# Optimization experiments

Hardware: AMD Instinct MI355X
Metric: run time of the kernel (lower is better)

The kernel has to match this reference:

```python
import jax, jax.numpy as jnp
import numpy as np

VERY_SMOL_NUM = -1e9  # undefined global in source; interpreted as large negative mask value
D_K = 128


def setup_inputs() -> dict:
    key = jax.random.key(0)
    k1, k2, k3 = jax.random.split(key, 3)
    B, S, D = 16, 2048, D_K
    Q = jax.random.normal(k1, (B, S, D), dtype=jnp.float32)
    K = jax.random.normal(k2, (B, S, D), dtype=jnp.float32)
    V = jax.random.normal(k3, (B, S, D), dtype=jnp.float32)
    return {"Q": Q, "K": K, "V": V}


def reference(Q, K, V):
    B, S, d_k = Q.shape
    # scores: [B, S, S] = Q @ K^T, scaled by 1/sqrt(d_k)
    x = jnp.einsum("bqd,bkd->bqk", Q, K) / jnp.sqrt(jnp.asarray(d_k, Q.dtype))
    # mask() is called unconditionally in the source (masked=False -> applied once):
    # add strict upper-triangular VERY_SMOL_NUM
    tri = jnp.triu(jnp.ones((S, S), dtype=x.dtype), k=1) * jnp.asarray(VERY_SMOL_NUM, x.dtype)
    x = x + tri  # broadcasts over batch, matching torch.triu on full shape
    # Softmax over dim=1 (query axis), as in the source (torch.nn.Softmax(dim=1))
    x = jax.nn.softmax(x, axis=1)
    return jnp.einsum("bqk,bkd->bqd", x, V)
```

## Files before the change

### kernel.cpp

```cpp
#include <hip/hip_runtime.h>


#define B_ 16
#define S_ 2048
#define D_ 128
#define QSCALE 0.12751744416825963f
#define NEG_BIG -1e30f
#define NCH 16
#define CHQ 128
#define PB 2162688

#define ROWW 136
#define P2RW 24

#define LDS_BARRIER()                                  \
  do {                                                 \
    asm volatile("s_waitcnt lgkmcnt(0)" ::: "memory"); \
    __builtin_amdgcn_s_barrier();                      \
  } while (0)

typedef short bf16x8 __attribute__((ext_vector_type(8)));
typedef float f32x4 __attribute__((ext_vector_type(4)));
typedef unsigned short u16x4 __attribute__((ext_vector_type(4)));
typedef unsigned int u32x2 __attribute__((ext_vector_type(2)));

#if defined(__has_builtin)
#if __has_builtin(__builtin_amdgcn_exp2f)
#define EXP2F(x) __builtin_amdgcn_exp2f(x)
#endif
#endif
#ifndef EXP2F
extern "C" __device__ float __ocml_exp2_f32(float);
#define EXP2F(x) __ocml_exp2_f32(x)
#endif

static __device__ __forceinline__ unsigned short f2bf(float f) {
  unsigned int u = __builtin_bit_cast(unsigned int, f);
  u += 0x7FFFu + ((u >> 16) & 1u);
  return (unsigned short)(u >> 16);
}

__global__ __launch_bounds__(256) void sdpa_convert(
    const float* __restrict__ Qr, const float* __restrict__ Kr,
    unsigned short* __restrict__ Qb, unsigned short* __restrict__ Kb) {
  const size_t t = (size_t)blockIdx.x * 256 + threadIdx.x;
  const float* src = blockIdx.y ? Kr : Qr;
  unsigned short* dstp = blockIdx.y ? Kb : Qb;
  const float sc = blockIdx.y ? 1.0f : QSCALE;
  f32x4 x = ((const f32x4*)src)[t];
  u16x4 o;
#pragma unroll
  for (int j = 0; j < 4; ++j) o[j] = f2bf(x[j] * sc);
  ((u16x4*)dstp)[t] = o;
}

__global__ __launch_bounds__(256, 4) void sdpa_pass1(
    const short* __restrict__ Qb, const short* __restrict__ Kb,
    float* __restrict__ lp_ws, unsigned short* __restrict__ Pt) {
  const int bid = blockIdx.x;
  int j = bid >> 4;
  int g = 0;
  while (j >= NCH - g) {
    j -= NCH - g;
    ++g;
  }
  const int ci = g + j;
  const int b = (bid & 7) + 8 * ((bid >> 3) & 1);

  __shared__ __align__(16) short Qst[2][32 * ROWW];
  const int tid = threadIdx.x;
  const int w = tid >> 6, lane = tid & 63, quad = lane >> 4, l15 = lane & 15;
  const int gg = 2 * g + (w >> 1);
  const int gb = 64 * gg;
  const int kb = gb + (w & 1) * 32;

  const size_t koff = ((size_t)b * S_ + kb + l15) * D_ + quad * 8;
  bf16x8 kh0[4], kh1[4];
#pragma unroll
  for (int c = 0; c < 4; ++c) {
    kh0[c] = *(const bf16x8*)(Kb + koff + c * 32);
    kh1[c] = *(const bf16x8*)(Kb + koff + 16 * D_ + c * 32);
  }

  const int nrp = S_ - gb;
  const size_t grp =
      (size_t)4 * ((size_t)gg * S_ - (size_t)(32 * gg) * (gg - 1));
  unsigned short* pw0 = Pt + (size_t)b * PB +
                        16 * (grp + (size_t)(2 * (w & 1)) * nrp) + quad * 4;
  unsigned short* pw1 = pw0 + (size_t)16 * nrp;

  const int sr = tid >> 3, sseg = tid & 7;
  const int q_start = CHQ * ci;

  {
    const short* sq = Qb + ((size_t)(b * S_ + q_start + sr)) * D_ + sseg * 16;
    bf16x8 h0 = *(const bf16x8*)(sq), h1 = *(const bf16x8*)(sq + 8);
    short* dst = &Qst[0][sr * ROWW + sseg * 16];
    *(bf16x8*)(dst) = h0;
    *(bf16x8*)(dst + 8) = h1;
  }
  LDS_BARRIER();

#define EMIT(q0s_, ktb_, cA_, pw_, lp_)                                       \
  do {                                                                        \
    float s0_ = cA_[0], s1_ = cA_[1], s2_ = cA_[2], s3_ = cA_[3];             \
    if ((q0s_) < (ktb_) + 16) {              \
      const int q_ = (q0s_) + l15;                                            \
      if ((ktb_) + quad * 4 + 0 > q_) s0_ = NEG_BIG;                          \
      if ((ktb_) + quad * 4 + 1 > q_) s1_ = NEG_BIG;                          \
      if ((ktb_) + quad * 4 + 2 > q_) s2_ = NEG_BIG;                          \
      if ((ktb_) + quad * 4 + 3 > q_) s3_ = NEG_BIG;                          \
    }                                                                         \
    const float e0_ = EXP2F(s0_), e1_ = EXP2F(s1_);                           \
    const float e2_ = EXP2F(s2_), e3_ = EXP2F(s3_);                           \
    lp_[0] += e0_;                                                            \
    lp_[1] += e1_;                                                            \
    lp_[2] += e2_;                                                            \
    lp_[3] += e3_;                                                            \
    unsigned int w0_, w1_;                                                    \
    asm("v_cvt_pk_bf16_f32 %0, %1, %2" : "=v"(w0_) : "v"(e0_), "v"(e1_));     \
    asm("v_cvt_pk_bf16_f32 %0, %1, %2" : "=v"(w1_) : "v"(e2_), "v"(e3_));     \
    u32x2 pk2_ = {w0_, w1_};                                                  \
    *(u32x2*)((pw_) + (size_t)((q0s_)-gb + l15) * 16) = pk2_;                 \
  } while (0)

  f32x4 lp0 = {0.f, 0.f, 0.f, 0.f}, lp1 = {0.f, 0.f, 0.f, 0.f};
#pragma unroll
  for (int it = 0; it < 4; ++it) {
    const int q0 = q_start + it * 32;
    const int cur = it & 1;
    bf16x8 h0, h1;
    if (it < 3) {
      const short* sq =
          Qb + ((size_t)(b * S_ + q0 + 32 + sr)) * D_ + sseg * 16;
      h0 = *(const bf16x8*)(sq);
      h1 = *(const bf16x8*)(sq + 8);
    }
#pragma unroll
    for (int sub = 0; sub < 2; ++sub) {
      const int q0s = q0 + sub * 16;
      if (q0s >= gb) {
        const short* rowp = &Qst[cur][(sub * 16 + l15) * ROWW + quad * 8];
        bf16x8 q0v = *(const bf16x8*)(rowp);
        bf16x8 q1v = *(const bf16x8*)(rowp + 32);
        bf16x8 q2v = *(const bf16x8*)(rowp + 64);
        bf16x8 q3v = *(const bf16x8*)(rowp + 96);
        f32x4 c0 = {0.f, 0.f, 0.f, 0.f};
        f32x4 c1 = {0.f, 0.f, 0.f, 0.f};
        c0 = __builtin_amdgcn_mfma_f32_16x16x32_bf16(kh0[0], q0v, c0, 0, 0, 0);
        c1 = __builtin_amdgcn_mfma_f32_16x16x32_bf16(kh1[0], q0v, c1, 0, 0, 0);
        c0 = __builtin_amdgcn_mfma_f32_16x16x32_bf16(kh0[1], q1v, c0, 0, 0, 0);
        c1 = __builtin_amdgcn_mfma_f32_16x16x32_bf16(kh1[1], q1v, c1, 0, 0, 0);
        c0 = __builtin_amdgcn_mfma_f32_16x16x32_bf16(kh0[2], q2v, c0, 0, 0, 0);
        c1 = __builtin_amdgcn_mfma_f32_16x16x32_bf16(kh1[2], q2v, c1, 0, 0, 0);
        c0 = __builtin_amdgcn_mfma_f32_16x16x32_bf16(kh0[3], q3v, c0, 0, 0, 0);
        c1 = __builtin_amdgcn_mfma_f32_16x16x32_bf16(kh1[3], q3v, c1, 0, 0, 0);
        EMIT(q0s, kb, c0, pw0, lp0);
        EMIT(q0s, kb + 16, c1, pw1, lp1);
      }
    }
    if (it < 3) {
      short* dst = &Qst[1 - cur][sr * ROWW + sseg * 16];
      *(bf16x8*)(dst) = h0;
      *(bf16x8*)(dst + 8) = h1;
    }
    LDS_BARRIER();
  }
#undef EMIT

#pragma unroll
  for (int d = 1; d < 16; d <<= 1) {
#pragma unroll
    for (int r = 0; r < 4; ++r) {
      lp0[r] += __shfl_xor(lp0[r], d, 64);
      lp1[r] += __shfl_xor(lp1[r], d, 64);
    }
  }
  if (l15 == 0) {
    float* dst = lp_ws + ((size_t)b * NCH + ci) * S_ + kb;
    *(f32x4*)(dst + quad * 4) = lp0;
    *(f32x4*)(dst + 16 + quad * 4) = lp1;
  }
}

__global__ __launch_bounds__(256) void sdpa_vscale(
    const float* __restrict__ Vr, const float* __restrict__ lp_ws,
    unsigned short* __restrict__ Vf) {
  __shared__ float Vld[32][132];
  __shared__ float as[32];
  const int kt = blockIdx.x, b = blockIdx.y, tid = threadIdx.x;
  const int k0 = kt * 32;
  const int row = tid >> 3, seg = tid & 7;
  const float* src = Vr + ((size_t)(b * S_ + k0 + row)) * D_ + seg * 16;
#pragma unroll
  for (int j = 0; j < 4; ++j) {
    f32x4 x = *(const f32x4*)(src + 4 * j);
    *(f32x4*)&Vld[row][seg * 16 + 4 * j] = x;
  }
  if (tid < 32) {
    const int k = k0 + tid;
    const int first = k >> 7;
    float l = 0.f;
#pragma unroll
    for (int ci = 0; ci < NCH; ++ci)
      if (ci >= first) l += lp_ws[((size_t)b * NCH + ci) * S_ + k];
    as[tid] = 1.0f / l;
  }
  __syncthreads();
  unsigned short* dst = Vf + ((size_t)(b * 64 + kt)) * 4096 + (size_t)tid * 16;
#pragma unroll
  for (int i = 0; i < 2; ++i) {
    const int u = tid * 2 + i;
    const int dt = u >> 6, l15 = (u >> 2) & 15, quad = u & 3;
    bf16x8 o;
#pragma unroll
    for (int e = 0; e < 8; ++e) {
      const int k = quad * 8 + e;
      o[e] = (short)f2bf(Vld[k][dt * 16 + l15] * as[k]);
    }
    *(bf16x8*)(dst + i * 8) = o;
  }
}

__global__ __launch_bounds__(512, 2) void sdpa_pass2(
    const unsigned short* __restrict__ Pt,
    const unsigned short* __restrict__ Vf, float* __restrict__ Out) {
  __shared__ __align__(16) short Pst[2][4 * 64 * P2RW];
  __shared__ __align__(16) short Vst[2][8192];
  const int bid = blockIdx.x;
  const int b = (bid & 7) + 8 * ((bid >> 3) & 1);
  const int py = bid >> 4;
  const int tid = threadIdx.x;
  const int w = tid >> 6, lane = tid & 63, quad = lane >> 4, l15 = lane & 15;
  const int qh = w & 3;
  const int dh = w >> 2;

  const int sp = tid >> 7, su = tid & 127, srow = su >> 1, sh = su & 1;

  const int ard = ((quad >> 1) * 64 + 16 * qh + l15) * P2RW + (quad & 1) * 8;
  const int awr = (sp * 64 + srow) * P2RW + sh * 8;
  const int vrd = dh * 2048 + l15 * 32 + quad * 8;

#define PLOAD(bx_, tp_, R_)                                                \
  do {                                                                     \
    const int pitch_ = 16 * (S_ - 64 * (tp_));                             \
    const unsigned short* g_ = Pt + (size_t)b * PB +                       \
                               2048 * (tp_) * (65 - (tp_)) + sp * pitch_ + \
                               (64 * ((bx_) - (tp_)) + srow) * 16 + sh * 8; \
    R_ = *(const bf16x8*)g_;                                               \
  } while (0)

#define VSLOAD(tp_, R_)                                                    \
  do {                                                                     \
    const unsigned short* g_ = Vf + (size_t)b * (64 * 4096) +              \
                               (size_t)(2 * (tp_)) * 4096 + tid * 8;       \
    R_[0] = *(const bf16x8*)g_;                                            \
    R_[1] = *(const bf16x8*)(g_ + 4096);                                   \
  } while (0)

#define WRITE_P(buf_, R_) *(bf16x8*)&Pst[buf_][awr] = R_

#define WRITE_V(buf_, R_)                           \
  do {                                              \
    *(bf16x8*)&Vst[buf_][tid * 8] = R_[0];          \
    *(bf16x8*)&Vst[buf_][4096 + tid * 8] = R_[1];   \
  } while (0)

#define COMPUTE(buf_)                                                        \
  do {                                                                       \
    bf16x8 A0 = *(const bf16x8*)&Pst[buf_][ard];                             \
    bf16x8 A1 = *(const bf16x8*)&Pst[buf_][ard + 2 * 64 * P2RW];             \
    _Pragma("unroll") for (int d_ = 0; d_ < 4; ++d_) {                       \
      bf16x8 v0_ = *(const bf16x8*)&Vst[buf_][vrd + d_ * 512];               \
      bf16x8 v1_ = *(const bf16x8*)&Vst[buf_][4096 + vrd + d_ * 512];        \
      acc[d_] = __builtin_amdgcn_mfma_f32_16x16x32_bf16(A0, v0_, acc[d_],    \
                                                        0, 0, 0);            \
      acc[d_] = __builtin_amdgcn_mfma_f32_16x16x32_bf16(A1, v1_, acc[d_],    \
                                                        0, 0, 0);            \
    }                                                                        \
  } while (0)

#pragma unroll
  for (int ti = 0; ti < 2; ++ti) {
    const int bx = ti ? (31 - py) : py;
    const int count = bx + 1;
    f32x4 acc[4];
#pragma unroll
    for (int d = 0; d < 4; ++d) acc[d] = (f32x4){0.f, 0.f, 0.f, 0.f};

    bf16x8 sP0, sP1, sV0[2], sV1[2];
    __builtin_amdgcn_s_barrier();
    PLOAD(bx, 0, sP0);
    VSLOAD(0, sV0);
    WRITE_P(0, sP0);
    WRITE_V(0, sV0);
    if (count > 1) {
      PLOAD(bx, 1, sP0);
      VSLOAD(1, sV0);
    }
    if (count > 2) {
      PLOAD(bx, 2, sP1);
      VSLOAD(2, sV1);
    }
    LDS_BARRIER();

    int tp = 0;
    while (tp + 2 <= count) {
      const int cur = tp & 1;
      {
        WRITE_P(cur ^ 1, sP0);
        WRITE_V(cur ^ 1, sV0);
        if (tp + 3 < count) {
          PLOAD(bx, tp + 3, sP0);
          VSLOAD(tp + 3, sV0);
        }
        COMPUTE(cur);
        LDS_BARRIER();
      }
      {
        if (tp + 2 < count) {
          WRITE_P(cur, sP1);
          WRITE_V(cur, sV1);
        }
        if (tp + 4 < count) {
          PLOAD(bx, tp + 4, sP1);
          VSLOAD(tp + 4, sV1);
        }
        COMPUTE(cur ^ 1);
        LDS_BARRIER();
      }
      tp += 2;
    }
    if (tp < count) {
      COMPUTE(tp & 1);
    }

    const int qw = 64 * bx + 16 * qh;
#pragma unroll
    for (int r = 0; r < 4; ++r) {
      float* op =
          Out + ((size_t)b * S_ + qw + quad * 4 + r) * D_ + dh * 64 + l15;
#pragma unroll
      for (int d = 0; d < 4; ++d) op[d * 16] = acc[d][r];
    }
  }
#undef PLOAD
#undef VSLOAD
#undef WRITE_P
#undef WRITE_V
#undef COMPUTE
}

extern "C" void kernel_launch(void* const* d_in, const int* in_sizes, int n_in,
                              void* d_out, int out_size, void* d_ws,
                              size_t ws_size, hipStream_t stream) {
  char* wsp = (char*)d_ws;
  float* lp_ws = (float*)wsp;
  char* p = wsp + (2 << 20);
  const size_t TSZ = (size_t)B_ * S_ * D_ * 2;
  unsigned short* Qb = (unsigned short*)(p);
  unsigned short* Kb = (unsigned short*)(p + TSZ);
  unsigned short* Vf = (unsigned short*)(p + 2 * TSZ);
  unsigned short* Pt = (unsigned short*)(p + 3 * TSZ);

  sdpa_convert<<<dim3((B_ * S_ * D_ / 4) / 256, 2), 256, 0, stream>>>(
      (const float*)d_in[0], (const float*)d_in[1], Qb, Kb);
  sdpa_pass1<<<dim3(NCH * 136), 256, 0, stream>>>(
      (const short*)Qb, (const short*)Kb, lp_ws, Pt);
  sdpa_vscale<<<dim3(S_ / 32, B_), 256, 0, stream>>>((const float*)d_in[2],
                                                     lp_ws, Vf);
  sdpa_pass2<<<dim3(256), 512, 0, stream>>>(Pt, Vf, (float*)d_out);
}
```

Measured before the change: 140.9 us.

## Pack two query chunks per 512-thread block in pass1

Each pass1 block now runs 512 threads, and each 256-thread half handles a different query chunk for the same key group. This halves the grid from 2176 to 1152 blocks and lets both halves share scheduling. Where the chunk count is odd, a half is inactive and skips its loads and compute but still joins the barriers. The change trades fewer, larger blocks and some idle half-blocks against lower per-block launch overhead. It also raises LDS use per block.

```diff
diff --git a/kernel.cpp b/kernel.cpp
--- a/kernel.cpp
+++ b/kernel.cpp
@@ -54,48 +54,54 @@
   ((u16x4*)dstp)[t] = o;
 }
 
-__global__ __launch_bounds__(256, 4) void sdpa_pass1(
+__global__ __launch_bounds__(512, 2) void sdpa_pass1(
     const short* __restrict__ Qb, const short* __restrict__ Kb,
     float* __restrict__ lp_ws, unsigned short* __restrict__ Pt) {
   const int bid = blockIdx.x;
   int j = bid >> 4;
   int g = 0;
-  while (j >= NCH - g) {
-    j -= NCH - g;
+  while (j >= ((NCH + 1 - g) >> 1)) {
+    j -= (NCH + 1 - g) >> 1;
     ++g;
   }
-  const int ci = g + j;
   const int b = (bid & 7) + 8 * ((bid >> 3) & 1);
 
-  __shared__ __align__(16) short Qst[2][32 * ROWW];
+  __shared__ __align__(16) short Qst[2][2][32 * ROWW];
   const int tid = threadIdx.x;
-  const int w = tid >> 6, lane = tid & 63, quad = lane >> 4, l15 = lane & 15;
-  const int gg = 2 * g + (w >> 1);
+  const int half = tid >> 8;
+  const int t8 = tid & 255;
+  const int wl = t8 >> 6, lane = tid & 63, quad = lane >> 4, l15 = lane & 15;
+  const int ci = g + 2 * j + half;
+  const bool act = (ci < NCH);
+
+  const int gg = 2 * g + (wl >> 1);
   const int gb = 64 * gg;
-  const int kb = gb + (w & 1) * 32;
+  const int kb = gb + (wl & 1) * 32;
 
   const size_t koff = ((size_t)b * S_ + kb + l15) * D_ + quad * 8;
   bf16x8 kh0[4], kh1[4];
-#pragma unroll
-  for (int c = 0; c < 4; ++c) {
-    kh0[c] = *(const bf16x8*)(Kb + koff + c * 32);
-    kh1[c] = *(const bf16x8*)(Kb + koff + 16 * D_ + c * 32);
+  if (act) {
+#pragma unroll
+    for (int c = 0; c < 4; ++c) {
+      kh0[c] = *(const bf16x8*)(Kb + koff + c * 32);
+      kh1[c] = *(const bf16x8*)(Kb + koff + 16 * D_ + c * 32);
+    }
   }
 
   const int nrp = S_ - gb;
   const size_t grp =
       (size_t)4 * ((size_t)gg * S_ - (size_t)(32 * gg) * (gg - 1));
   unsigned short* pw0 = Pt + (size_t)b * PB +
-                        16 * (grp + (size_t)(2 * (w & 1)) * nrp) + quad * 4;
+                        16 * (grp + (size_t)(2 * (wl & 1)) * nrp) + quad * 4;
   unsigned short* pw1 = pw0 + (size_t)16 * nrp;
 
-  const int sr = tid >> 3, sseg = tid & 7;
+  const int sr = t8 >> 3, sseg = t8 & 7;
   const int q_start = CHQ * ci;
 
-  {
+  if (act) {
     const short* sq = Qb + ((size_t)(b * S_ + q_start + sr)) * D_ + sseg * 16;
     bf16x8 h0 = *(const bf16x8*)(sq), h1 = *(const bf16x8*)(sq + 8);
-    short* dst = &Qst[0][sr * ROWW + sseg * 16];
+    short* dst = &Qst[half][0][sr * ROWW + sseg * 16];
     *(bf16x8*)(dst) = h0;
     *(bf16x8*)(dst + 8) = h1;
   }
@@ -130,56 +136,61 @@
     const int q0 = q_start + it * 32;
     const int cur = it & 1;
     bf16x8 h0, h1;
-    if (it < 3) {
+    if (act && it < 3) {
       const short* sq =
           Qb + ((size_t)(b * S_ + q0 + 32 + sr)) * D_ + sseg * 16;
       h0 = *(const bf16x8*)(sq);
       h1 = *(const bf16x8*)(sq + 8);
     }
-#pragma unroll
-    for (int sub = 0; sub < 2; ++sub) {
-      const int q0s = q0 + sub * 16;
-      if (q0s >= gb) {
-        const short* rowp = &Qst[cur][(sub * 16 + l15) * ROWW + quad * 8];
-        bf16x8 q0v = *(const bf16x8*)(rowp);
-        bf16x8 q1v = *(const bf16x8*)(rowp + 32);
-        bf16x8 q2v = *(const bf16x8*)(rowp + 64);
-        bf16x8 q3v = *(const bf16x8*)(rowp + 96);
-        f32x4 c0 = {0.f, 0.f, 0.f, 0.f};
-        f32x4 c1 = {0.f, 0.f, 0.f, 0.f};
-        c0 = __builtin_amdgcn_mfma_f32_16x16x32_bf16(kh0[0], q0v, c0, 0, 0, 0);
-        c1 = __builtin_amdgcn_mfma_f32_16x16x32_bf16(kh1[0], q0v, c1, 0, 0, 0);
-        c0 = __builtin_amdgcn_mfma_f32_16x16x32_bf16(kh0[1], q1v, c0, 0, 0, 0);
-        c1 = __builtin_amdgcn_mfma_f32_16x16x32_bf16(kh1[1], q1v, c1, 0, 0, 0);
-        c0 = __builtin_amdgcn_mfma_f32_16x16x32_bf16(kh0[2], q2v, c0, 0, 0, 0);
-        c1 = __builtin_amdgcn_mfma_f32_16x16x32_bf16(kh1[2], q2v, c1, 0, 0, 0);
-        c0 = __builtin_amdgcn_mfma_f32_16x16x32_bf16(kh0[3], q3v, c0, 0, 0, 0);
-        c1 = __builtin_amdgcn_mfma_f32_16x16x32_bf16(kh1[3], q3v, c1, 0, 0, 0);
-        EMIT(q0s, kb, c0, pw0, lp0);
-        EMIT(q0s, kb + 16, c1, pw1, lp1);
-      }
-    }
-    if (it < 3) {
-      short* dst = &Qst[1 - cur][sr * ROWW + sseg * 16];
-      *(bf16x8*)(dst) = h0;
-      *(bf16x8*)(dst + 8) = h1;
+    if (act) {
+#pragma unroll
+      for (int sub = 0; sub < 2; ++sub) {
+        const int q0s = q0 + sub * 16;
+        if (q0s >= gb) {
+          const short* rowp =
+              &Qst[half][cur][(sub * 16 + l15) * ROWW + quad * 8];
+          bf16x8 q0v = *(const bf16x8*)(rowp);
+          bf16x8 q1v = *(const bf16x8*)(rowp + 32);
+          bf16x8 q2v = *(const bf16x8*)(rowp + 64);
+          bf16x8 q3v = *(const bf16x8*)(rowp + 96);
+          f32x4 c0 = {0.f, 0.f, 0.f, 0.f};
+          f32x4 c1 = {0.f, 0.f, 0.f, 0.f};
+          c0 = __builtin_amdgcn_mfma_f32_16x16x32_bf16(kh0[0], q0v, c0, 0, 0, 0);
+          c1 = __builtin_amdgcn_mfma_f32_16x16x32_bf16(kh1[0], q0v, c1, 0, 0, 0);
+          c0 = __builtin_amdgcn_mfma_f32_16x16x32_bf16(kh0[1], q1v, c0, 0, 0, 0);
+          c1 = __builtin_amdgcn_mfma_f32_16x16x32_bf16(kh1[1], q1v, c1, 0, 0, 0);
+          c0 = __builtin_amdgcn_mfma_f32_16x16x32_bf16(kh0[2], q2v, c0, 0, 0, 0);
+          c1 = __builtin_amdgcn_mfma_f32_16x16x32_bf16(kh1[2], q2v, c1, 0, 0, 0);
+          c0 = __builtin_amdgcn_mfma_f32_16x16x32_bf16(kh0[3], q3v, c0, 0, 0, 0);
+          c1 = __builtin_amdgcn_mfma_f32_16x16x32_bf16(kh1[3], q3v, c1, 0, 0, 0);
+          EMIT(q0s, kb, c0, pw0, lp0);
+          EMIT(q0s, kb + 16, c1, pw1, lp1);
+        }
+      }
+      if (it < 3) {
+        short* dst = &Qst[half][1 - cur][sr * ROWW + sseg * 16];
+        *(bf16x8*)(dst) = h0;
+        *(bf16x8*)(dst + 8) = h1;
+      }
     }
     LDS_BARRIER();
   }
 #undef EMIT
 
-#pragma unroll
-  for (int d = 1; d < 16; d <<= 1) {
-#pragma unroll
-    for (int r = 0; r < 4; ++r) {
-      lp0[r] += __shfl_xor(lp0[r], d, 64);
-      lp1[r] += __shfl_xor(lp1[r], d, 64);
-    }
-  }
-  if (l15 == 0) {
-    float* dst = lp_ws + ((size_t)b * NCH + ci) * S_ + kb;
-    *(f32x4*)(dst + quad * 4) = lp0;
-    *(f32x4*)(dst + 16 + quad * 4) = lp1;
+  if (act) {
+#pragma unroll
+    for (int d = 1; d < 16; d <<= 1) {
+#pragma unroll
+      for (int r = 0; r < 4; ++r) {
+        lp0[r] += __shfl_xor(lp0[r], d, 64);
+        lp1[r] += __shfl_xor(lp1[r], d, 64);
+      }
+    }
+    if (l15 == 0) {
+      float* dst = lp_ws + ((size_t)b * NCH + ci) * S_ + kb;
+      *(f32x4*)(dst + quad * 4) = lp0;
+      *(f32x4*)(dst + 16 + quad * 4) = lp1;
+    }
   }
 }
 
@@ -365,7 +376,7 @@
 
   sdpa_convert<<<dim3((B_ * S_ * D_ / 4) / 256, 2), 256, 0, stream>>>(
       (const float*)d_in[0], (const float*)d_in[1], Qb, Kb);
-  sdpa_pass1<<<dim3(NCH * 136), 256, 0, stream>>>(
+  sdpa_pass1<<<dim3(16 * 72), 512, 0, stream>>>(
       (const short*)Qb, (const short*)Kb, lp_ws, Pt);
   sdpa_vscale<<<dim3(S_ / 32, B_), 256, 0, stream>>>((const float*)d_in[2],
                                                      lp_ws, Vf);
```

Measured after the change: 146.1 us. +3.7%, slower.
